# Kernel optimization log

Hardware: AMD Instinct MI355X
Metric: run time of the kernel (lower is better)

Reference implementation:

```python
import jax, jax.numpy as jnp
import numpy as np

HEADS = 4
REDUCTION = 4
BN_EPS = 1e-5


def conv1x1_bn(x, W, b, gamma, beta, mean, var):
    # x: [B, C, W, H]; 1x1 conv == channel matmul, then BN (inference form)
    y = jnp.einsum('oc,bcwh->bowh', W, x) + b[None, :, None, None]
    scale = (gamma / jnp.sqrt(var + BN_EPS))[None, :, None, None]
    return (y - mean[None, :, None, None]) * scale + beta[None, :, None, None]


def setup_inputs() -> dict:
    key = jax.random.key(0)
    ks = jax.random.split(key, 24)
    C, Cq = 512, 512 // REDUCTION  # 128
    B, Wd, Hd = 16, 32, 32
    dh = Cq // HEADS  # 32
    rnd = lambda k, s: jax.random.normal(k, s, dtype=jnp.float32)
    pos = lambda k, s: jax.random.uniform(k, s, dtype=jnp.float32, minval=0.5, maxval=1.5)
    return {
        'x': rnd(ks[0], (B, C, Wd, Hd)),
        'Wq': rnd(ks[1], (Cq, C)) * 0.05, 'bq': rnd(ks[2], (Cq,)) * 0.05,
        'q_gamma': pos(ks[3], (Cq,)), 'q_beta': rnd(ks[4], (Cq,)) * 0.05,
        'q_mean': rnd(ks[5], (Cq,)) * 0.05, 'q_var': pos(ks[6], (Cq,)),
        'Wk': rnd(ks[7], (Cq, C)) * 0.05, 'bk': rnd(ks[8], (Cq,)) * 0.05,
        'k_gamma': pos(ks[9], (Cq,)), 'k_beta': rnd(ks[10], (Cq,)) * 0.05,
        'k_mean': rnd(ks[11], (Cq,)) * 0.05, 'k_var': pos(ks[12], (Cq,)),
        'Wv': rnd(ks[13], (C, C)) * 0.05, 'bv': rnd(ks[14], (C,)) * 0.05,
        'v_gamma': pos(ks[15], (C,)), 'v_beta': rnd(ks[16], (C,)) * 0.05,
        'v_mean': rnd(ks[17], (C,)) * 0.05, 'v_var': pos(ks[18], (C,)),
        'rel_h': rnd(ks[19], (1, HEADS, dh, 1, Hd)),
        'rel_w': rnd(ks[20], (1, HEADS, dh, Wd, 1)),
    }


def reference(x, Wq, bq, q_gamma, q_beta, q_mean, q_var,
              Wk, bk, k_gamma, k_beta, k_mean, k_var,
              Wv, bv, v_gamma, v_beta, v_mean, v_var,
              rel_h, rel_w):
    B, C, Wd, Hd = x.shape
    N = Wd * Hd
    dh = C // REDUCTION // HEADS
    dv = C // HEADS
    q = conv1x1_bn(x, Wq, bq, q_gamma, q_beta, q_mean, q_var).reshape(B, HEADS, dh, N)
    k = conv1x1_bn(x, Wk, bk, k_gamma, k_beta, k_mean, k_var).reshape(B, HEADS, dh, N)
    v = conv1x1_bn(x, Wv, bv, v_gamma, v_beta, v_mean, v_var).reshape(B, HEADS, dv, N)
    # content-content: q^T k -> [B, H, N, N]
    cc = jnp.einsum('bhdn,bhdm->bhnm', q, k)
    # content-position: (rel_h + rel_w) flattened to [H, dh, N], then pos^T @ q
    pos = (rel_h + rel_w).reshape(HEADS, dh, N)
    cp = jnp.einsum('hdn,bhdm->bhnm', pos, q)
    attn = jax.nn.softmax(cc + cp, axis=-1)
    # out = v @ attn^T  (torch: matmul(v, attention.permute(0,1,3,2)))
    out = jnp.einsum('bhcn,bhmn->bhcm', v, attn)
    return out.reshape(B, C, Wd, Hd) + x
```

## Files before the change

### kernel.cpp

```cpp
#include <hip/hip_runtime.h>


typedef _Float16 f16x8 __attribute__((ext_vector_type(8)));
typedef __attribute__((ext_vector_type(4))) float f32x4;
typedef __attribute__((ext_vector_type(4))) unsigned int u32x4;
typedef __attribute__((ext_vector_type(2))) unsigned int u32x2;

#define MFMAH(a, b, c) __builtin_amdgcn_mfma_f32_16x16x32_f16(a, b, c, 0, 0, 0)
#define LOG2E 1.4426950408889634f

__device__ __forceinline__ unsigned pkh(float a, float b) {
  auto p = __builtin_amdgcn_cvt_pkrtz(a, b);
  return __builtin_bit_cast(unsigned, p);
}
__device__ __forceinline__ short f2h(float a) {
  _Float16 h = (_Float16)a;
  return __builtin_bit_cast(short, h);
}

__device__ __forceinline__ void gload16(const void* g, void* l) {
  __builtin_amdgcn_global_load_lds(
      (const __attribute__((address_space(1))) void*)g,
      (__attribute__((address_space(3))) void*)l, 16, 0, 0);
}

__global__ __launch_bounds__(256) void setup_kernel(
    const float* __restrict__ Wq, const float* __restrict__ bq,
    const float* __restrict__ qg, const float* __restrict__ qbe,
    const float* __restrict__ qme, const float* __restrict__ qva,
    const float* __restrict__ Wk, const float* __restrict__ bk,
    const float* __restrict__ kg, const float* __restrict__ kbe,
    const float* __restrict__ kme, const float* __restrict__ kva,
    const float* __restrict__ Wv, const float* __restrict__ bv,
    const float* __restrict__ vg, const float* __restrict__ vbe,
    const float* __restrict__ vme, const float* __restrict__ vva,
    const float* __restrict__ rel_h, const float* __restrict__ rel_w,
    unsigned short* __restrict__ Wh, float* __restrict__ bfv,
    unsigned short* __restrict__ posH)
{
  int bid = blockIdx.x;
  if (bid < 1536) {
    int idx = bid * 256 + threadIdx.x;
    if (idx >= 768 * 512) return;
    int o = idx >> 9, c = idx & 511;
    float w, sc, bb, mean, beta, post;
    if (o < 128) {
      sc = qg[o] / sqrtf(qva[o] + 1e-5f);
      w = Wq[o * 512 + c]; bb = bq[o]; mean = qme[o]; beta = qbe[o];
      post = LOG2E;
    } else if (o < 256) {
      int r = o - 128;
      sc = kg[r] / sqrtf(kva[r] + 1e-5f);
      w = Wk[r * 512 + c]; bb = bk[r]; mean = kme[r]; beta = kbe[r];
      post = 1.0f;
    } else {
      int r = o - 256;
      sc = vg[r] / sqrtf(vva[r] + 1e-5f);
      w = Wv[r * 512 + c]; bb = bv[r]; mean = vme[r]; beta = vbe[r];
      post = 1.0f;
    }
    Wh[idx] = (unsigned short)f2h(w * sc * post);
    if (c == 0) bfv[o] = ((bb - mean) * sc + beta) * post;
  } else {
    int idx = (bid - 1536) * 256 + threadIdx.x;
    if (idx >= 4 * 1024 * 32) return;
    int h = idx >> 15, rem = idx & 32767, n = rem >> 5, d = rem & 31;
    int w = n >> 5, hh = n & 31;
    float v = rel_h[(h * 32 + d) * 32 + hh] + rel_w[(h * 32 + d) * 32 + w];
    posH[idx] = (unsigned short)f2h(v);
  }
}

__global__ __launch_bounds__(512) void proj_kernel(
    const float* __restrict__ x,
    const unsigned short* __restrict__ Wh, const float* __restrict__ bfv,
    unsigned short* __restrict__ qH, unsigned short* __restrict__ kH,
    unsigned short* __restrict__ vH)
{
  __shared__ __align__(16) short sm[16384];

  int bid = blockIdx.x;
  int b = bid / 48, rem = bid % 48, mblk = rem >> 3, nblk = rem & 7;
  int Mb = mblk * 128, Nb = nblk * 128;
  int t = threadIdx.x;
  int lane = t & 63, w = t >> 6, ln = lane & 15, g = (lane >> 4) & 3;
  int wm = w >> 2, wn = w & 3;
  int kg8 = t >> 6, np = t & 63;
  int n0 = 2 * np;
  int swp = (np >> 2) & 1;

  f32x4 acc[4][2];
  for (int i = 0; i < 4; i++)
    for (int j = 0; j < 2; j++) acc[i][j] = (f32x4){0.f, 0.f, 0.f, 0.f};

  for (int kb = 0; kb < 512; kb += 64) {
    __syncthreads();
    for (int i = 0; i < 2; i++) {
      int grp = w + i * 8;
      int unit = grp * 64 + lane;
      int row = unit >> 3, pos = unit & 7;
      int j = pos ^ (row & 7);
      gload16(&Wh[(Mb + row) * 512 + kb + j * 8], &sm[grp * 512]);
    }
    {
      float2 fB[8];
      for (int rr = 0; rr < 8; rr++)
        fB[rr] = *(const float2*)&x[(b * 512 + kb + kg8 * 8 + rr) * 1024 +
                                    Nb + n0];
      short* Bt = sm + 8192;
      u32x4 wE = (u32x4){pkh(fB[0].x, fB[1].x), pkh(fB[2].x, fB[3].x),
                         pkh(fB[4].x, fB[5].x), pkh(fB[6].x, fB[7].x)};
      u32x4 wO = (u32x4){pkh(fB[0].y, fB[1].y), pkh(fB[2].y, fB[3].y),
                         pkh(fB[4].y, fB[5].y), pkh(fB[6].y, fB[7].y)};
      int offE = n0 * 64 + 8 * (kg8 ^ (n0 & 7));
      int offO = (n0 + 1) * 64 + 8 * (kg8 ^ ((n0 + 1) & 7));
      int o1 = swp ? offO : offE, o2 = swp ? offE : offO;
      u32x4 d1 = swp ? wO : wE, d2 = swp ? wE : wO;
      *(u32x4*)&Bt[o1] = d1;
      *(u32x4*)&Bt[o2] = d2;
    }
    __syncthreads();

    const short* Bt = sm + 8192;
    for (int ks = 0; ks < 2; ks++) {
      f16x8 af[4], bf[2];
      for (int mt = 0; mt < 4; mt++) {
        int o = wm * 64 + mt * 16 + ln;
        af[mt] = *(const f16x8*)&sm[o * 64 + 8 * ((ks * 4 + g) ^ (o & 7))];
      }
      for (int nt = 0; nt < 2; nt++) {
        int n = wn * 32 + nt * 16 + ln;
        bf[nt] = *(const f16x8*)&Bt[n * 64 + 8 * ((ks * 4 + g) ^ (n & 7))];
      }
      __builtin_amdgcn_s_setprio(1);
      for (int mt = 0; mt < 4; mt++)
        for (int nt = 0; nt < 2; nt++)
          acc[mt][nt] = MFMAH(af[mt], bf[nt], acc[mt][nt]);
      __builtin_amdgcn_s_setprio(0);
    }
  }

  unsigned* smU = (unsigned*)sm;
  for (int p = 0; p < 2; p++) {
    __syncthreads();
    if ((wn >> 1) == p) {
      if (mblk < 2) {
        for (int mt = 0; mt < 4; mt++)
          for (int nt = 0; nt < 2; nt++) {
            float y0 = acc[mt][nt][0] + bfv[Mb + wm * 64 + mt * 16 + g * 4 + 0];
            float y1 = acc[mt][nt][1] + bfv[Mb + wm * 64 + mt * 16 + g * 4 + 1];
            float y2 = acc[mt][nt][2] + bfv[Mb + wm * 64 + mt * 16 + g * 4 + 2];
            float y3 = acc[mt][nt][3] + bfv[Mb + wm * 64 + mt * 16 + g * 4 + 3];
            u32x2 pk = (u32x2){pkh(y0, y1), pkh(y2, y3)};
            int nl = (wn & 1) * 32 + nt * 16 + ln;
            *(u32x2*)&smU[nl * 66 + wm * 32 + mt * 8 + g * 2] = pk;
          }
      } else {
        for (int mt = 0; mt < 4; mt++)
          for (int nt = 0; nt < 2; nt++)
            for (int r = 0; r < 4; r++) {
              int o = wm * 64 + mt * 16 + g * 4 + r;
              sm[o * 72 + (wn & 1) * 32 + nt * 16 + ln] =
                  f2h(acc[mt][nt][r] + bfv[Mb + o]);
            }
      }
    }
    __syncthreads();
    if (mblk < 2) {
      unsigned short* dh = (mblk == 0) ? qH : kH;
      for (int it = 0; it < 2; it++) {
        int task = it * 512 + t;
        int h = task >> 8, nl = (task >> 2) & 63, qc = task & 3;
        u32x4 v4 = *(const u32x4*)&smU[nl * 66 + h * 16 + qc * 4];
        int gi = ((b * 4 + h) * 1024 + Nb + p * 64 + nl) * 32 + qc * 8;
        *(u32x4*)&dh[gi] = v4;
      }
    } else {
      int bh = b * 4 + (mblk - 2);
      for (int it = 0; it < 2; it++) {
        int task = it * 512 + t;
        int o = task >> 3, qc = task & 7;
        u32x4 vv = *(const u32x4*)&sm[o * 72 + qc * 8];
        *(u32x4*)&vH[(bh * 128 + o) * 1024 + Nb + p * 64 + qc * 8] = vv;
      }
    }
  }
}

__global__ __launch_bounds__(512, 4) void attn_kernel(
    const float* __restrict__ x,
    const unsigned short* __restrict__ qH, const unsigned short* __restrict__ kH,
    const unsigned short* __restrict__ posH, const unsigned short* __restrict__ vH,
    float* __restrict__ out)
{
  __shared__ __align__(16) short sm[2 * 12288];

  int bid = blockIdx.x;
  int bh = (bid & 7) * 8 + ((bid >> 3) & 7);
  int qt = bid >> 6;
  int b = bh >> 2, h = bh & 3;
  int t = threadIdx.x;
  int lane = t & 63, w = t >> 6, ln = lane & 15, g = (lane >> 4) & 3;

  int qrow = qt * 128 + w * 16 + ln;
  f16x8 bQ   = *(const f16x8*)&qH[(bh * 1024 + qrow) * 32 + g * 8];
  f16x8 bPos = *(const f16x8*)&posH[(h * 1024 + qrow) * 32 + g * 8];

  f16x8 aOnes;
  {
    _Float16 o1 = (ln == 0) ? (_Float16)1.0f : (_Float16)0.0f;
    for (int i = 0; i < 8; i++) aOnes[i] = o1;
  }

  f32x4 acc[9];
  for (int ct = 0; ct < 9; ct++) acc[ct] = (f32x4){0.f, 0.f, 0.f, 0.f};
  float m_run = -1e30f;

  int addr0 = ((((2 * g) & 3) * 16) + ln) * 4;
  int addr1 = ((((2 * g + 1) & 3) * 16) + ln) * 4;

  int uK = t & 255;
  int rK = uK >> 2;
  int chK = (uK & 3) ^ (rK & 3) ^ ((rK >> 2) & 3);
  const unsigned short* pKQ =
      ((t < 256) ? kH : qH) + (long)(bh * 1024 + rK) * 32 + chK * 8;
  int ldsKQ = ((t < 256) ? 0 : 2048) + (w & 3) * 512;
  int c0 = t >> 3, vch0 = (t & 7) ^ (c0 & 7);
  int u1 = t + 512, c1 = u1 >> 3, vch1 = (u1 & 7) ^ (c1 & 7);
  const unsigned short* pV0 = vH + (long)(bh * 128 + c0) * 1024 + vch0 * 8;
  const unsigned short* pV1 = vH + (long)(bh * 128 + c1) * 1024 + vch1 * 8;
  int ldsV0 = 4096 + w * 512;
  int ldsV1 = 4096 + (w + 8) * 512;

  auto STAGE = [&](int bb, int jb) {
    int base = bb * 12288;
    gload16(pKQ + (long)jb * 32, &sm[base + ldsKQ]);
    gload16(pV0 + jb, &sm[base + ldsV0]);
    gload16(pV1 + jb, &sm[base + ldsV1]);
  };

  STAGE(0, 0);

  for (int it = 0; it < 16; ++it) {
    int cur = it & 1;
    if (it < 15) {
      STAGE(cur ^ 1, (it + 1) * 64);
      asm volatile("s_waitcnt vmcnt(3)" ::: "memory");
    } else {
      asm volatile("s_waitcnt vmcnt(0)" ::: "memory");
    }
    __builtin_amdgcn_s_barrier();
    __builtin_amdgcn_sched_barrier(0);

    const short* B = &sm[cur * 12288];

    f16x8 aK[4], aQ[4];
    for (int kt = 0; kt < 4; kt++) {
      int r = kt * 16 + ln;
      int p = g ^ (r & 3) ^ ((r >> 2) & 3);
      int off = r * 32 + p * 8;
      aK[kt] = *(const f16x8*)&B[off];
      aQ[kt] = *(const f16x8*)&B[2048 + off];
    }

    f32x4 s[4];
    for (int kt = 0; kt < 4; kt++) s[kt] = (f32x4){0.f, 0.f, 0.f, 0.f};
    __builtin_amdgcn_s_setprio(1);
    for (int kt = 0; kt < 4; kt++) s[kt] = MFMAH(aK[kt], bQ, s[kt]);
    for (int kt = 0; kt < 4; kt++) s[kt] = MFMAH(aQ[kt], bPos, s[kt]);
    __builtin_amdgcn_s_setprio(0);

    float m0 = fmaxf(fmaxf(s[0][0], s[0][1]), fmaxf(s[0][2], s[0][3]));
    float m1 = fmaxf(fmaxf(s[1][0], s[1][1]), fmaxf(s[1][2], s[1][3]));
    float m2 = fmaxf(fmaxf(s[2][0], s[2][1]), fmaxf(s[2][2], s[2][3]));
    float m3 = fmaxf(fmaxf(s[3][0], s[3][1]), fmaxf(s[3][2], s[3][3]));
    float mx = fmaxf(fmaxf(m0, m1), fmaxf(m2, m3));
    if (__any(mx > m_run + 8.f)) {
      float mxf = fmaxf(mx, __shfl_xor(mx, 16));
      mxf = fmaxf(mxf, __shfl_xor(mxf, 32));
      float mnew = fmaxf(m_run, mxf);
      float scl = __builtin_amdgcn_exp2f(m_run - mnew);
      for (int ct = 0; ct < 9; ct++) acc[ct] *= scl;
      m_run = mnew;
    }
    for (int kt = 0; kt < 4; kt++)
      for (int r = 0; r < 4; r++)
        s[kt][r] = __builtin_amdgcn_exp2f(s[kt][r] - m_run);

    unsigned pw[8];
#pragma unroll
    for (int kt = 0; kt < 4; kt++) {
      pw[kt * 2 + 0] = pkh(s[kt][0], s[kt][1]);
      pw[kt * 2 + 1] = pkh(s[kt][2], s[kt][3]);
    }

    f16x8 pFrag[2];
#pragma unroll
    for (int st2 = 0; st2 < 2; st2++) {
      unsigned wd[4];
#pragma unroll
      for (int u = 0; u < 4; u++) {
        int a = (u >> 1) ? addr1 : addr0;
        unsigned lo = pw[4 * st2 + (u & 1)];
        unsigned hi = pw[4 * st2 + 2 + (u & 1)];
        unsigned v0 = (unsigned)__builtin_amdgcn_ds_bpermute(a, (int)lo);
        unsigned v1 = (unsigned)__builtin_amdgcn_ds_bpermute(a, (int)hi);
        wd[u] = (g < 2) ? v0 : v1;
      }
      union { u32x4 u4; f16x8 v8; } cv;
      cv.u4 = (u32x4){wd[0], wd[1], wd[2], wd[3]};
      pFrag[st2] = cv.v8;
    }

    __builtin_amdgcn_s_setprio(1);
    for (int ct = 0; ct < 8; ct++)
      for (int st2 = 0; st2 < 2; st2++) {
        int c = ct * 16 + ln;
        int pos = (st2 * 4 + g) ^ (c & 7);
        f16x8 av = *(const f16x8*)&B[4096 + c * 64 + pos * 8];
        acc[ct] = MFMAH(av, pFrag[st2], acc[ct]);
      }
    acc[8] = MFMAH(aOnes, pFrag[0], acc[8]);
    acc[8] = MFMAH(aOnes, pFrag[1], acc[8]);
    __builtin_amdgcn_s_setprio(0);

    __builtin_amdgcn_sched_barrier(0);
    __builtin_amdgcn_s_barrier();
    __builtin_amdgcn_sched_barrier(0);
  }

  float lsum = __shfl(acc[8][0], ln);
  float inv = 1.0f / lsum;
  int m = qt * 128 + w * 16 + ln;
  for (int ct = 0; ct < 8; ct++)
    for (int r = 0; r < 4; r++) {
      int c = h * 128 + ct * 16 + g * 4 + r;
      int gi = (b * 512 + c) * 1024 + m;
      out[gi] = acc[ct][r] * inv + x[gi];
    }
}

extern "C" void kernel_launch(void* const* d_in, const int* in_sizes, int n_in,
                              void* d_out, int out_size, void* d_ws, size_t ws_size,
                              hipStream_t stream) {
  const float* x    = (const float*)d_in[0];
  const float* Wq   = (const float*)d_in[1];
  const float* bq   = (const float*)d_in[2];
  const float* qg   = (const float*)d_in[3];
  const float* qbe  = (const float*)d_in[4];
  const float* qme  = (const float*)d_in[5];
  const float* qva  = (const float*)d_in[6];
  const float* Wk   = (const float*)d_in[7];
  const float* bk   = (const float*)d_in[8];
  const float* kg   = (const float*)d_in[9];
  const float* kbe  = (const float*)d_in[10];
  const float* kme  = (const float*)d_in[11];
  const float* kva  = (const float*)d_in[12];
  const float* Wv   = (const float*)d_in[13];
  const float* bv   = (const float*)d_in[14];
  const float* vg   = (const float*)d_in[15];
  const float* vbe  = (const float*)d_in[16];
  const float* vme  = (const float*)d_in[17];
  const float* vva  = (const float*)d_in[18];
  const float* relh = (const float*)d_in[19];
  const float* relw = (const float*)d_in[20];
  float* outp = (float*)d_out;

  unsigned char* ws = (unsigned char*)d_ws;
  unsigned short* Whp  = (unsigned short*)(ws + 0);
  float*          bfv  = (float*)(ws + 786432);
  unsigned short* qHp  = (unsigned short*)(ws + 789504);
  unsigned short* kHp  = (unsigned short*)(ws + 4983808);
  unsigned short* posHp= (unsigned short*)(ws + 9178112);
  unsigned short* vHp  = (unsigned short*)(ws + 9440256);

  setup_kernel<<<2048, 256, 0, stream>>>(Wq, bq, qg, qbe, qme, qva,
                                         Wk, bk, kg, kbe, kme, kva,
                                         Wv, bv, vg, vbe, vme, vva,
                                         relh, relw, Whp, bfv, posHp);
  proj_kernel<<<768, 512, 0, stream>>>(x, Whp, bfv, qHp, kHp, vHp);
  attn_kernel<<<512, 512, 0, stream>>>(x, qHp, kHp, posHp, vHp, outp);
}
```

Measured before the change: 80.80 us.

## Switch attention kernel to 32x32x16 MFMA tiles with permlane-based P transpose

```diff
diff --git a/kernel.cpp b/kernel.cpp
--- a/kernel.cpp
+++ b/kernel.cpp
@@ -3,10 +3,12 @@
 
 typedef _Float16 f16x8 __attribute__((ext_vector_type(8)));
 typedef __attribute__((ext_vector_type(4))) float f32x4;
+typedef __attribute__((ext_vector_type(16))) float f32x16;
 typedef __attribute__((ext_vector_type(4))) unsigned int u32x4;
 typedef __attribute__((ext_vector_type(2))) unsigned int u32x2;
 
 #define MFMAH(a, b, c) __builtin_amdgcn_mfma_f32_16x16x32_f16(a, b, c, 0, 0, 0)
+#define MFMA32(a, b, c) __builtin_amdgcn_mfma_f32_32x32x16_f16(a, b, c, 0, 0, 0)
 #define LOG2E 1.4426950408889634f
 
 __device__ __forceinline__ unsigned pkh(float a, float b) {
@@ -200,35 +202,35 @@
   int qt = bid >> 6;
   int b = bh >> 2, h = bh & 3;
   int t = threadIdx.x;
-  int lane = t & 63, w = t >> 6, ln = lane & 15, g = (lane >> 4) & 3;
-
-  int qrow = qt * 128 + w * 16 + ln;
-  f16x8 bQ   = *(const f16x8*)&qH[(bh * 1024 + qrow) * 32 + g * 8];
-  f16x8 bPos = *(const f16x8*)&posH[(h * 1024 + qrow) * 32 + g * 8];
-
-  f16x8 aOnes;
-  {
-    _Float16 o1 = (ln == 0) ? (_Float16)1.0f : (_Float16)0.0f;
-    for (int i = 0; i < 8; i++) aOnes[i] = o1;
-  }
-
-  f32x4 acc[9];
-  for (int ct = 0; ct < 9; ct++) acc[ct] = (f32x4){0.f, 0.f, 0.f, 0.f};
-  float m_run = -1e30f;
-
-  int addr0 = ((((2 * g) & 3) * 16) + ln) * 4;
-  int addr1 = ((((2 * g + 1) & 3) * 16) + ln) * 4;
-
-  int uK = t & 255;
-  int rK = uK >> 2;
-  int chK = (uK & 3) ^ (rK & 3) ^ ((rK >> 2) & 3);
+  int lane = t & 63, w = t >> 6;
+  int ln32 = lane & 31, hi = lane >> 5;
+  int grp = w & 3, chalf = w >> 2;
+
+  int qrow = qt * 128 + grp * 32 + ln32;
+  f16x8 bQ[2], bPos[2];
+#pragma unroll
+  for (int dblk = 0; dblk < 2; dblk++) {
+    bQ[dblk]   = *(const f16x8*)&qH[(bh * 1024 + qrow) * 32 + dblk * 16 + hi * 8];
+    bPos[dblk] = *(const f16x8*)&posH[(h * 1024 + qrow) * 32 + dblk * 16 + hi * 8];
+  }
+
+  f32x16 acc0, acc1;
+#pragma unroll
+  for (int r = 0; r < 16; r++) { acc0[r] = 0.f; acc1[r] = 0.f; }
+  float m_run = -1e30f, l_run = 0.f;
+
+  int uR = t & 255;
+  int rowK = uR >> 2, posK = uR & 3;
+  int chK = posK ^ ((rowK >> 3) & 3);
   const unsigned short* pKQ =
-      ((t < 256) ? kH : qH) + (long)(bh * 1024 + rK) * 32 + chK * 8;
-  int ldsKQ = ((t < 256) ? 0 : 2048) + (w & 3) * 512;
-  int c0 = t >> 3, vch0 = (t & 7) ^ (c0 & 7);
-  int u1 = t + 512, c1 = u1 >> 3, vch1 = (u1 & 7) ^ (c1 & 7);
-  const unsigned short* pV0 = vH + (long)(bh * 128 + c0) * 1024 + vch0 * 8;
-  const unsigned short* pV1 = vH + (long)(bh * 128 + c1) * 1024 + vch1 * 8;
+      ((t < 256) ? kH : qH) + (long)(bh * 1024 + rowK) * 32 + chK * 8;
+  int ldsKQ = w * 512;
+  int cV0 = t >> 3, sV0 = t & 7;
+  int chV0 = sV0 ^ ((cV0 >> 2) & 7);
+  const unsigned short* pV0 = vH + (long)(bh * 128 + cV0) * 1024 + chV0 * 8;
+  int u1 = t + 512, cV1 = u1 >> 3, sV1 = u1 & 7;
+  int chV1 = sV1 ^ ((cV1 >> 2) & 7);
+  const unsigned short* pV1 = vH + (long)(bh * 128 + cV1) * 1024 + chV1 * 8;
   int ldsV0 = 4096 + w * 512;
   int ldsV1 = 4096 + (w + 8) * 512;
 
@@ -254,74 +256,92 @@
 
     const short* B = &sm[cur * 12288];
 
-    f16x8 aK[4], aQ[4];
-    for (int kt = 0; kt < 4; kt++) {
-      int r = kt * 16 + ln;
-      int p = g ^ (r & 3) ^ ((r >> 2) & 3);
-      int off = r * 32 + p * 8;
-      aK[kt] = *(const f16x8*)&B[off];
-      aQ[kt] = *(const f16x8*)&B[2048 + off];
-    }
-
-    f32x4 s[4];
-    for (int kt = 0; kt < 4; kt++) s[kt] = (f32x4){0.f, 0.f, 0.f, 0.f};
+    f32x16 sc0, sc1;
+#pragma unroll
+    for (int r = 0; r < 16; r++) { sc0[r] = 0.f; sc1[r] = 0.f; }
     __builtin_amdgcn_s_setprio(1);
-    for (int kt = 0; kt < 4; kt++) s[kt] = MFMAH(aK[kt], bQ, s[kt]);
-    for (int kt = 0; kt < 4; kt++) s[kt] = MFMAH(aQ[kt], bPos, s[kt]);
+#pragma unroll
+    for (int dblk = 0; dblk < 2; dblk++) {
+      int chunk = dblk * 2 + hi;
+      {
+        int j = ln32;
+        int off = j * 32 + (chunk ^ ((j >> 3) & 3)) * 8;
+        f16x8 aK  = *(const f16x8*)&B[off];
+        f16x8 aQk = *(const f16x8*)&B[2048 + off];
+        sc0 = MFMA32(aK, bQ[dblk], sc0);
+        sc0 = MFMA32(aQk, bPos[dblk], sc0);
+      }
+      {
+        int j = 32 + ln32;
+        int off = j * 32 + (chunk ^ ((j >> 3) & 3)) * 8;
+        f16x8 aK  = *(const f16x8*)&B[off];
+        f16x8 aQk = *(const f16x8*)&B[2048 + off];
+        sc1 = MFMA32(aK, bQ[dblk], sc1);
+        sc1 = MFMA32(aQk, bPos[dblk], sc1);
+      }
+    }
     __builtin_amdgcn_s_setprio(0);
 
-    float m0 = fmaxf(fmaxf(s[0][0], s[0][1]), fmaxf(s[0][2], s[0][3]));
-    float m1 = fmaxf(fmaxf(s[1][0], s[1][1]), fmaxf(s[1][2], s[1][3]));
-    float m2 = fmaxf(fmaxf(s[2][0], s[2][1]), fmaxf(s[2][2], s[2][3]));
-    float m3 = fmaxf(fmaxf(s[3][0], s[3][1]), fmaxf(s[3][2], s[3][3]));
-    float mx = fmaxf(fmaxf(m0, m1), fmaxf(m2, m3));
+    float mA = -1e30f, mB = -1e30f;
+#pragma unroll
+    for (int r = 0; r < 16; r += 2) {
+      mA = fmaxf(mA, fmaxf(sc0[r], sc0[r + 1]));
+      mB = fmaxf(mB, fmaxf(sc1[r], sc1[r + 1]));
+    }
+    float mx = fmaxf(mA, mB);
     if (__any(mx > m_run + 8.f)) {
-      float mxf = fmaxf(mx, __shfl_xor(mx, 16));
-      mxf = fmaxf(mxf, __shfl_xor(mxf, 32));
+      float mxf = fmaxf(mx, __shfl_xor(mx, 32));
       float mnew = fmaxf(m_run, mxf);
       float scl = __builtin_amdgcn_exp2f(m_run - mnew);
-      for (int ct = 0; ct < 9; ct++) acc[ct] *= scl;
+#pragma unroll
+      for (int r = 0; r < 16; r++) { acc0[r] *= scl; acc1[r] *= scl; }
+      l_run *= scl;
       m_run = mnew;
     }
-    for (int kt = 0; kt < 4; kt++)
-      for (int r = 0; r < 4; r++)
-        s[kt][r] = __builtin_amdgcn_exp2f(s[kt][r] - m_run);
-
-    unsigned pw[8];
-#pragma unroll
-    for (int kt = 0; kt < 4; kt++) {
-      pw[kt * 2 + 0] = pkh(s[kt][0], s[kt][1]);
-      pw[kt * 2 + 1] = pkh(s[kt][2], s[kt][3]);
-    }
-
-    f16x8 pFrag[2];
-#pragma unroll
-    for (int st2 = 0; st2 < 2; st2++) {
-      unsigned wd[4];
-#pragma unroll
-      for (int u = 0; u < 4; u++) {
-        int a = (u >> 1) ? addr1 : addr0;
-        unsigned lo = pw[4 * st2 + (u & 1)];
-        unsigned hi = pw[4 * st2 + 2 + (u & 1)];
-        unsigned v0 = (unsigned)__builtin_amdgcn_ds_bpermute(a, (int)lo);
-        unsigned v1 = (unsigned)__builtin_amdgcn_ds_bpermute(a, (int)hi);
-        wd[u] = (g < 2) ? v0 : v1;
-      }
+#pragma unroll
+    for (int r = 0; r < 16; r++) {
+      sc0[r] = __builtin_amdgcn_exp2f(sc0[r] - m_run);
+      sc1[r] = __builtin_amdgcn_exp2f(sc1[r] - m_run);
+    }
+    float rs = 0.f;
+#pragma unroll
+    for (int r = 0; r < 16; r += 4) {
+      rs += ((sc0[r] + sc0[r + 1]) + (sc0[r + 2] + sc0[r + 3]));
+      rs += ((sc1[r] + sc1[r + 1]) + (sc1[r + 2] + sc1[r + 3]));
+    }
+    rs += __shfl_xor(rs, 32);
+    l_run += rs;
+
+    unsigned pw[16];
+#pragma unroll
+    for (int p2 = 0; p2 < 8; p2++) {
+      pw[p2]     = pkh(sc0[2 * p2], sc0[2 * p2 + 1]);
+      pw[8 + p2] = pkh(sc1[2 * p2], sc1[2 * p2 + 1]);
+    }
+    f16x8 bP[4];
+#pragma unroll
+    for (int kc = 0; kc < 4; kc++) {
+      int bse = kc * 4;
+      unsigned w0 = pw[bse + 0], w2 = pw[bse + 2];
+      unsigned w1 = pw[bse + 1], w3 = pw[bse + 3];
+      asm("v_permlane32_swap_b32 %0, %1" : "+v"(w0), "+v"(w2));
+      asm("v_permlane32_swap_b32 %0, %1" : "+v"(w1), "+v"(w3));
       union { u32x4 u4; f16x8 v8; } cv;
-      cv.u4 = (u32x4){wd[0], wd[1], wd[2], wd[3]};
-      pFrag[st2] = cv.v8;
+      cv.u4 = (u32x4){w0, w1, w2, w3};
+      bP[kc] = cv.v8;
     }
 
     __builtin_amdgcn_s_setprio(1);
-    for (int ct = 0; ct < 8; ct++)
-      for (int st2 = 0; st2 < 2; st2++) {
-        int c = ct * 16 + ln;
-        int pos = (st2 * 4 + g) ^ (c & 7);
-        f16x8 av = *(const f16x8*)&B[4096 + c * 64 + pos * 8];
-        acc[ct] = MFMAH(av, pFrag[st2], acc[ct]);
-      }
-    acc[8] = MFMAH(aOnes, pFrag[0], acc[8]);
-    acc[8] = MFMAH(aOnes, pFrag[1], acc[8]);
+#pragma unroll
+    for (int kc = 0; kc < 4; kc++) {
+      int chunk = kc * 2 + hi;
+      int c = chalf * 64 + ln32;
+      f16x8 aV = *(const f16x8*)&B[4096 + c * 64 + (chunk ^ ((c >> 2) & 7)) * 8];
+      acc0 = MFMA32(aV, bP[kc], acc0);
+      int c2 = c + 32;
+      f16x8 aV2 = *(const f16x8*)&B[4096 + c2 * 64 + (chunk ^ ((c2 >> 2) & 7)) * 8];
+      acc1 = MFMA32(aV2, bP[kc], acc1);
+    }
     __builtin_amdgcn_s_setprio(0);
 
     __builtin_amdgcn_sched_barrier(0);
@@ -329,15 +349,17 @@
     __builtin_amdgcn_sched_barrier(0);
   }
 
-  float lsum = __shfl(acc[8][0], ln);
-  float inv = 1.0f / lsum;
-  int m = qt * 128 + w * 16 + ln;
-  for (int ct = 0; ct < 8; ct++)
-    for (int r = 0; r < 4; r++) {
-      int c = h * 128 + ct * 16 + g * 4 + r;
-      int gi = (b * 512 + c) * 1024 + m;
-      out[gi] = acc[ct][r] * inv + x[gi];
-    }
+  float inv = 1.0f / l_run;
+  int q = qt * 128 + grp * 32 + ln32;
+#pragma unroll
+  for (int r = 0; r < 16; r++) {
+    int crow = (r & 3) + 8 * (r >> 2) + 4 * hi;
+    int c = h * 128 + chalf * 64 + crow;
+    int gi = (b * 512 + c) * 1024 + q;
+    out[gi] = acc0[r] * inv + x[gi];
+    int gi2 = gi + 32 * 1024;
+    out[gi2] = acc1[r] * inv + x[gi2];
+  }
 }
 
 extern "C" void kernel_launch(void* const* d_in, const int* in_sizes, int n_in,
```

New measurement: 96.15 us. 1.19x slower.
